# Kernel tuning notes

Measured on AMD Instinct MI355X. Metric: run time of the kernel, lower is better.

Reference implementation:

```python
import jax, jax.numpy as jnp
import numpy as np

N, E, F, H, D, C = 50000, 800000, 128, 8, 16, 40


def setup_inputs() -> dict:
    key = jax.random.key(0)
    ks = jax.random.split(key, 12)
    s_in = 1.0 / np.sqrt(F)
    s_h = 1.0 / np.sqrt(H * D)
    return {
        "x": jax.random.normal(ks[0], (N, F), jnp.float32),
        "edge_index": jax.random.randint(ks[1], (2, E), 0, N, jnp.int64),
        "W1": jax.random.normal(ks[2], (F, H * D), jnp.float32) * s_in,
        "a_src1": jax.random.normal(ks[3], (H, D), jnp.float32) * s_h,
        "a_dst1": jax.random.normal(ks[4], (H, D), jnp.float32) * s_h,
        "b1": jnp.zeros((H * D,), jnp.float32),
        "W2": jax.random.normal(ks[5], (H * D, H * D), jnp.float32) * s_h,
        "a_src2": jax.random.normal(ks[6], (H, D), jnp.float32) * s_h,
        "a_dst2": jax.random.normal(ks[7], (H, D), jnp.float32) * s_h,
        "b2": jnp.zeros((H * D,), jnp.float32),
        "Wc": jax.random.normal(ks[8], (H * D, C), jnp.float32) * s_h,
        "bc": jnp.zeros((C,), jnp.float32),
    }


def _gat_layer(x, src, dst, W, a_src, a_dst, b):
    # x: [N, F_in]; src/dst: [E'] (self-loops already appended)
    n = x.shape[0]
    h, d = a_src.shape
    hx = (x @ W).reshape(n, h, d)                      # [N, H, D]
    al_src = jnp.einsum("nhd,hd->nh", hx, a_src)       # [N, H]
    al_dst = jnp.einsum("nhd,hd->nh", hx, a_dst)       # [N, H]
    e = jax.nn.leaky_relu(al_src[src] + al_dst[dst], 0.2)  # [E', H]
    # segment softmax over incoming edges of each destination node
    m = jax.ops.segment_max(e, dst, num_segments=n)    # [N, H]
    e = jnp.exp(e - m[dst])
    z = jax.ops.segment_sum(e, dst, num_segments=n)    # [N, H]
    alpha = e / z[dst]                                 # [E', H]
    out = jax.ops.segment_sum(alpha[:, :, None] * hx[src], dst, num_segments=n)
    return out.reshape(n, h * d) + b


def reference(x, edge_index, W1, a_src1, a_dst1, b1, W2, a_src2, a_dst2, b2, Wc, bc):
    n = x.shape[0]
    loops = jnp.arange(n, dtype=edge_index.dtype)
    src = jnp.concatenate([edge_index[0], loops])  # PyG GATConv adds self-loops
    dst = jnp.concatenate([edge_index[1], loops])
    h = _gat_layer(x, src, dst, W1, a_src1, a_dst1, b1)
    h = jax.nn.elu(h)  # ELU between layers (i < K-1); dropout=None -> no-op
    h = _gat_layer(h, src, dst, W2, a_src2, a_dst2, b2)
    return h @ Wc + bc  # [N, C] logits
```

## Files before the change

kernel.cpp:

```cpp
#include <hip/hip_runtime.h>
#include <hip/hip_bf16.h>


#define FDIM 128
#define HEADS 8

typedef short bf16x8 __attribute__((ext_vector_type(8)));
typedef float f32x4 __attribute__((ext_vector_type(4)));

__device__ __forceinline__ float leaky02(float x) {
    return fmaxf(x, 0.2f * x);
}

__device__ __forceinline__ unsigned pack2bf(float x, float y) {
    unsigned a = __float_as_uint(x), b = __float_as_uint(y);
    a += 0x7fffu + ((a >> 16) & 1u);
    b += 0x7fffu + ((b >> 16) & 1u);
    return (a >> 16) | (b & 0xffff0000u);
}

__device__ __forceinline__ void split2(float x, unsigned short& hi, unsigned short& lo) {
    unsigned bits = __float_as_uint(x);
    unsigned h = bits + 0x7fffu + ((bits >> 16) & 1u);
    hi = (unsigned short)(h >> 16);
    float hf = __uint_as_float(h & 0xffff0000u);
    float r = x - hf;
    unsigned rb = __float_as_uint(r);
    unsigned l2 = rb + 0x7fffu + ((rb >> 16) & 1u);
    lo = (unsigned short)(l2 >> 16);
}


__global__ __launch_bounds__(256) void prep_kernel(const int* __restrict__ ei,
                                                   int* __restrict__ deg,
                                                   int* __restrict__ rank,
                                                   int E,
                                                   const float* __restrict__ x,
                                                   unsigned short* __restrict__ x_hi,
                                                   unsigned short* __restrict__ x_lo,
                                                   int nel,
                                                   const float* __restrict__ W1,
                                                   const float* __restrict__ W2,
                                                   unsigned short* __restrict__ w1_hi,
                                                   unsigned short* __restrict__ w1_lo,
                                                   unsigned short* __restrict__ w2_hi,
                                                   unsigned short* __restrict__ w2_lo,
                                                   int histB, int xB) {
    int b = blockIdx.x, t = threadIdx.x;
    if (b < histB) {
        int e = b * 256 + t;
        if (e < E) rank[e] = atomicAdd(&deg[ei[E + e]], 1);
        return;
    }
    b -= histB;
    if (b < xB) {
        int i0 = (b * 256 + t) * 8;
        if (i0 < nel) {
            float4 v0 = *(const float4*)&x[i0];
            float4 v1 = *(const float4*)&x[i0 + 4];
            float vv[8] = {v0.x, v0.y, v0.z, v0.w, v1.x, v1.y, v1.z, v1.w};
            unsigned short h[8], l[8];
#pragma unroll
            for (int j = 0; j < 8; ++j) split2(vv[j], h[j], l[j]);
            uint4 hh, ll;
            hh.x = h[0] | ((unsigned)h[1] << 16);
            hh.y = h[2] | ((unsigned)h[3] << 16);
            hh.z = h[4] | ((unsigned)h[5] << 16);
            hh.w = h[6] | ((unsigned)h[7] << 16);
            ll.x = l[0] | ((unsigned)l[1] << 16);
            ll.y = l[2] | ((unsigned)l[3] << 16);
            ll.z = l[4] | ((unsigned)l[5] << 16);
            ll.w = l[6] | ((unsigned)l[7] << 16);
            *(uint4*)&x_hi[i0] = hh;
            *(uint4*)&x_lo[i0] = ll;
        }
        return;
    }
    b -= xB;
    const float* W = (b < 16) ? W1 : W2;
    unsigned short* whi = (b < 16) ? w1_hi : w2_hi;
    unsigned short* wlo = (b < 16) ? w1_lo : w2_lo;
    int idx = (b & 15) * 256 + t;
    int k = idx >> 5;
    int c0 = (idx & 31) * 4;
#pragma unroll
    for (int i = 0; i < 4; ++i) {
        int c = c0 + i;
        float v = W[k * FDIM + c];
        unsigned short h, l;
        split2(v, h, l);
        int dest = ((k >> 5) * 8 + (c >> 4)) * 512 +
                   ((c & 15) + (((k >> 3) & 3) << 4)) * 8 + (k & 7);
        whi[dest] = h;
        wlo[dest] = l;
    }
}


__global__ __launch_bounds__(256) void scan_partial(const int* __restrict__ deg,
                                                    int* __restrict__ partials,
                                                    int n) {
    __shared__ int red[256];
    int t = threadIdx.x;
    int base = blockIdx.x * 1024 + t * 4;
    int s = 0;
#pragma unroll
    for (int j = 0; j < 4; ++j) {
        int i = base + j;
        if (i < n) s += deg[i];
    }
    red[t] = s;
    __syncthreads();
    for (int off = 128; off > 0; off >>= 1) {
        if (t < off) red[t] += red[t + off];
        __syncthreads();
    }
    if (t == 0) partials[blockIdx.x] = red[0];
}

__global__ __launch_bounds__(64) void scan_offsets(int* __restrict__ partials,
                                                   int* __restrict__ row_start,
                                                   int nb, int n) {
    int lane = threadIdx.x;
    int carry = 0;
    for (int base = 0; base < nb; base += 64) {
        int idx = base + lane;
        int v = (idx < nb) ? partials[idx] : 0;
        int incl = v;
#pragma unroll
        for (int off = 1; off < 64; off <<= 1) {
            int t = __shfl_up(incl, off);
            if (lane >= off) incl += t;
        }
        if (idx < nb) partials[idx] = carry + incl - v;
        carry += __shfl(incl, 63);
    }
    if (lane == 0) row_start[n] = carry;
}

__global__ __launch_bounds__(256) void scan_final(const int* __restrict__ deg,
                                                  const int* __restrict__ partials,
                                                  int* __restrict__ row_start,
                                                  int n) {
    __shared__ int sbuf[256];
    int t = threadIdx.x;
    int base = blockIdx.x * 1024 + t * 4;
    int v[4];
#pragma unroll
    for (int j = 0; j < 4; ++j) v[j] = (base + j < n) ? deg[base + j] : 0;
    int tsum = v[0] + v[1] + v[2] + v[3];
    sbuf[t] = tsum;
    __syncthreads();
    for (int off = 1; off < 256; off <<= 1) {
        int tmp = (t >= off) ? sbuf[t - off] : 0;
        __syncthreads();
        sbuf[t] += tmp;
        __syncthreads();
    }
    int toff = partials[blockIdx.x] + sbuf[t] - tsum;
    int run = 0;
#pragma unroll
    for (int j = 0; j < 4; ++j) {
        int i = base + j;
        if (i < n) row_start[i] = toff + run;
        run += v[j];
    }
}


template <bool SCATTER>
__global__ __launch_bounds__(256, 4) void gemm_mfma(const unsigned short* __restrict__ a_hi,
                                                    const unsigned short* __restrict__ a_lo,
                                                    const unsigned short* __restrict__ w_hi,
                                                    const unsigned short* __restrict__ w_lo,
                                                    const float* __restrict__ asrc,
                                                    const float* __restrict__ adst,
                                                    float* __restrict__ als,
                                                    float* __restrict__ ald,
                                                    unsigned* __restrict__ hxb,
                                                    int n,
                                                    const int* __restrict__ ei,
                                                    const int* __restrict__ rank,
                                                    const int* __restrict__ row_start,
                                                    int* __restrict__ csr_src,
                                                    int E, int ng, int grid) {
    int tid = threadIdx.x;
    int gb;
    if (SCATTER) {
        int bid = blockIdx.x;
        int t0 = (int)((long long)bid * ng / grid);
        int t1 = (int)((long long)(bid + 1) * ng / grid);
        if (t1 == t0) {
            int sb = bid - t0;
#pragma unroll
            for (int j = 0; j < 4; ++j) {
                int e = sb * 1024 + j * 256 + tid;
                if (e < E) {
                    int s = ei[e];
                    int d = ei[E + e];
                    csr_src[row_start[d] + rank[e]] = s;
                }
            }
            return;
        }
        gb = t0;
    } else {
        gb = blockIdx.x;
    }

    int lane = tid & 63;
    int wave = tid >> 6;
    int l15 = lane & 15;
    int lg = lane >> 4;
    int row0 = gb * 32;

    f32x4 acc[2][2];
#pragma unroll
    for (int fr = 0; fr < 2; ++fr)
#pragma unroll
        for (int fc = 0; fc < 2; ++fc)
#pragma unroll
            for (int r = 0; r < 4; ++r) acc[fr][fc][r] = 0.f;

#pragma unroll
    for (int kc = 0; kc < 4; ++kc) {
        bf16x8 Ah[2], Al[2], Bh[2], Bl[2];
#pragma unroll
        for (int fr = 0; fr < 2; ++fr) {
            int r = row0 + fr * 16 + l15;
            if (r > n - 1) r = n - 1;
            size_t off = (size_t)r * FDIM + kc * 32 + lg * 8;
            Ah[fr] = *(const bf16x8*)(a_hi + off);
            Al[fr] = *(const bf16x8*)(a_lo + off);
        }
#pragma unroll
        for (int fc = 0; fc < 2; ++fc) {
            int FC = wave * 2 + fc;
            size_t off = (size_t)(kc * 8 + FC) * 512 + lane * 8;
            Bh[fc] = *(const bf16x8*)(w_hi + off);
            Bl[fc] = *(const bf16x8*)(w_lo + off);
        }
#pragma unroll
        for (int fr = 0; fr < 2; ++fr)
#pragma unroll
            for (int fc = 0; fc < 2; ++fc) {
                acc[fr][fc] = __builtin_amdgcn_mfma_f32_16x16x32_bf16(
                    Al[fr], Bh[fc], acc[fr][fc], 0, 0, 0);
                acc[fr][fc] = __builtin_amdgcn_mfma_f32_16x16x32_bf16(
                    Ah[fr], Bl[fc], acc[fr][fc], 0, 0, 0);
                acc[fr][fc] = __builtin_amdgcn_mfma_f32_16x16x32_bf16(
                    Ah[fr], Bh[fc], acc[fr][fc], 0, 0, 0);
            }
    }

#pragma unroll
    for (int fr = 0; fr < 2; ++fr)
#pragma unroll
        for (int fc = 0; fc < 2; ++fc) {
            int CB = wave * 32 + fc * 16;
            int col = CB + l15;
            float as_ = asrc[col];
            float ad_ = adst[col];
#pragma unroll
            for (int reg = 0; reg < 4; ++reg) {
                int row = row0 + fr * 16 + lg * 4 + reg;
                float v = acc[fr][fc][reg];
                float vn = __shfl_xor(v, 1);
                if ((lane & 1) == 0 && row < n)
                    hxb[(size_t)row * 64 + (col >> 1)] = pack2bf(v, vn);
                float ps = v * as_;
                float pd = v * ad_;
                ps += __shfl_xor(ps, 1);
                pd += __shfl_xor(pd, 1);
                ps += __shfl_xor(ps, 2);
                pd += __shfl_xor(pd, 2);
                ps += __shfl_xor(ps, 4);
                pd += __shfl_xor(pd, 4);
                ps += __shfl_xor(ps, 8);
                pd += __shfl_xor(pd, 8);
                if (l15 == 0 && row < n) {
                    als[row * HEADS + (CB >> 4)] = ps;
                    ald[row * HEADS + (CB >> 4)] = pd;
                }
            }
        }
}


__global__ __launch_bounds__(256, 8) void gemm_cls(const unsigned* __restrict__ h_hi,
                                                   const unsigned* __restrict__ h_lo,
                                                   const float* __restrict__ W,
                                                   const float* __restrict__ bias,
                                                   float* __restrict__ out,
                                                   int n) {
    __shared__ float xs[32][136];
    __shared__ float ws[32][48];
    int tid = threadIdx.x;
    int row0 = blockIdx.x * 128;
    int lane = tid & 63;
    int wave = tid >> 6;
    int lane2 = lane * 2;
    int wc = wave * 10;

    float acc[2][10];
#pragma unroll
    for (int i = 0; i < 2; ++i)
#pragma unroll
        for (int j = 0; j < 10; ++j) acc[i][j] = 0.f;

    for (int kc = 0; kc < 128; kc += 32) {
        if (kc) __syncthreads();
#pragma unroll
        for (int it = 0; it < 4; ++it) {
            int idx = it * 256 + tid;
            int r = idx >> 3, kg = (idx & 7) * 4;
            float4 v = make_float4(0.f, 0.f, 0.f, 0.f);
            if (row0 + r < n) {
                uint2 hh = *(const uint2*)&h_hi[(size_t)(row0 + r) * 64 + (kc + kg) / 2];
                uint2 ll = *(const uint2*)&h_lo[(size_t)(row0 + r) * 64 + (kc + kg) / 2];
                v.x = __uint_as_float(hh.x << 16) + __uint_as_float(ll.x << 16);
                v.y = __uint_as_float(hh.x & 0xffff0000u) + __uint_as_float(ll.x & 0xffff0000u);
                v.z = __uint_as_float(hh.y << 16) + __uint_as_float(ll.y << 16);
                v.w = __uint_as_float(hh.y & 0xffff0000u) + __uint_as_float(ll.y & 0xffff0000u);
            }
            int col = r ^ kg;
            xs[kg + 0][col] = v.x;
            xs[kg + 1][col] = v.y;
            xs[kg + 2][col] = v.z;
            xs[kg + 3][col] = v.w;
        }
#pragma unroll
        for (int it = 0; it < 6; ++it) {
            int idx = it * 256 + tid;
            int kk = idx / 48, c = idx - kk * 48;
            ws[kk][c] = (c < 40) ? W[(size_t)(kc + kk) * 40 + c] : 0.f;
        }
        __syncthreads();
#pragma unroll
        for (int k = 0; k < 32; ++k) {
            int s = ((k >> 2) & 7) << 2;
            float2 av2 = *(const float2*)&xs[k][lane2 ^ s];
            float av[2] = {av2.x, av2.y};
#pragma unroll
            for (int j = 0; j < 10; ++j) {
                float w = ws[k][wc + j];
                acc[0][j] += av[0] * w;
                acc[1][j] += av[1] * w;
            }
        }
    }

#pragma unroll
    for (int i = 0; i < 2; ++i) {
        int row = row0 + lane2 + i;
        if (row < n) {
#pragma unroll
            for (int j = 0; j < 10; ++j)
                out[(size_t)row * 40 + wc + j] = acc[i][j] + bias[wc + j];
        }
    }
}


template <bool DOELU>
__global__ __launch_bounds__(256) void gat_aggregate(const unsigned* __restrict__ hxb,
                                                     const float* __restrict__ als,
                                                     const float* __restrict__ ald,
                                                     const int* __restrict__ row_start,
                                                     const int* __restrict__ csr_src,
                                                     const float* __restrict__ bias,
                                                     unsigned* __restrict__ h_hi,
                                                     unsigned* __restrict__ h_lo,
                                                     int n) {
    int wid = threadIdx.x >> 6;
    int lane = threadIdx.x & 63;
    int node = blockIdx.x * 4 + wid;
    if (node >= n) return;

    int rs = row_start[node];
    int deg = row_start[node + 1] - rs;

    int h = lane & 7;
    int hc = lane >> 3;
    float ald_h = ald[node * HEADS + h];

    float acc0 = 0.f, acc1 = 0.f, z = 0.f;
    int total = deg + 1;
    int i0 = 0;
    for (; i0 + 8 <= total; i0 += 8) {
        int ii = i0 + (lane >> 3);
        int srcv = (ii < deg) ? csr_src[rs + ii] : node;
        float w = __expf(leaky02(als[srcv * HEADS + h] + ald_h));
#pragma unroll
        for (int e = 0; e < 8; ++e) {
            int s    = __shfl(srcv, e * 8);
            float we = __shfl(w, e * 8 + hc);
            unsigned v = hxb[(size_t)s * 64 + lane];
            z += we;
            acc0 += we * __uint_as_float(v << 16);
            acc1 += we * __uint_as_float(v & 0xffff0000u);
        }
    }
    {
        int ii = i0 + (lane >> 3);
        int srcv = (ii < deg) ? csr_src[rs + ii] : node;
        float w = (ii < total) ? __expf(leaky02(als[srcv * HEADS + h] + ald_h)) : 0.f;
        int rem = total - i0;
        for (int e = 0; e < rem; ++e) {
            int s    = __shfl(srcv, e * 8);
            float we = __shfl(w, e * 8 + hc);
            unsigned v = hxb[(size_t)s * 64 + lane];
            z += we;
            acc0 += we * __uint_as_float(v << 16);
            acc1 += we * __uint_as_float(v & 0xffff0000u);
        }
    }

    float2 bv = *(const float2*)&bias[2 * lane];
    float o0 = acc0 / z + bv.x;
    float o1 = acc1 / z + bv.y;
    if (DOELU) {
        o0 = o0 > 0.f ? o0 : (__expf(o0) - 1.f);
        o1 = o1 > 0.f ? o1 : (__expf(o1) - 1.f);
    }
    unsigned short h0, l0, h1, l1;
    split2(o0, h0, l0);
    split2(o1, h1, l1);
    h_hi[(size_t)node * 64 + lane] = (unsigned)h0 | ((unsigned)h1 << 16);
    h_lo[(size_t)node * 64 + lane] = (unsigned)l0 | ((unsigned)l1 << 16);
}


extern "C" void kernel_launch(void* const* d_in, const int* in_sizes, int n_in,
                              void* d_out, int out_size, void* d_ws, size_t ws_size,
                              hipStream_t stream) {
    const float* x      = (const float*)d_in[0];
    const int*   ei     = (const int*)d_in[1];
    const float* W1     = (const float*)d_in[2];
    const float* a_src1 = (const float*)d_in[3];
    const float* a_dst1 = (const float*)d_in[4];
    const float* b1     = (const float*)d_in[5];
    const float* W2     = (const float*)d_in[6];
    const float* a_src2 = (const float*)d_in[7];
    const float* a_dst2 = (const float*)d_in[8];
    const float* b2     = (const float*)d_in[9];
    const float* Wc     = (const float*)d_in[10];
    const float* bc     = (const float*)d_in[11];
    float* out = (float*)d_out;

    const int N = in_sizes[0] / FDIM;
    const int E = in_sizes[1] / 2;
    const int NB = (N + 1023) / 1024;
    const int nel = N * FDIM;

    unsigned* hxb = (unsigned*)d_ws;
    unsigned* xh_u = hxb + (size_t)N * 64;
    unsigned* xl_u = xh_u + (size_t)N * 64;
    float* als  = (float*)(xl_u + (size_t)N * 64);
    float* ald  = als + (size_t)N * HEADS;
    unsigned short* w1_hi = (unsigned short*)(ald + (size_t)N * HEADS);
    unsigned short* w1_lo = w1_hi + 16384;
    unsigned short* w2_hi = w1_lo + 16384;
    unsigned short* w2_lo = w2_hi + 16384;
    int* deg       = (int*)(w2_lo + 16384);
    int* row_start = deg + N;
    int* partials  = row_start + ((N + 8) & ~3);
    int* rank      = partials + ((NB + 4) & ~3);
    int* csr_src   = rank + E;

    unsigned short* x_hi = (unsigned short*)xh_u;
    unsigned short* x_lo = (unsigned short*)xl_u;

    hipMemsetAsync(deg, 0, (size_t)N * sizeof(int), stream);
    const int histB = (E + 255) / 256;
    const int xB = (nel + 2047) / 2048;
    prep_kernel<<<histB + xB + 32, 256, 0, stream>>>(
        ei, deg, rank, E, x, x_hi, x_lo, nel,
        W1, W2, w1_hi, w1_lo, w2_hi, w2_lo, histB, xB);
    scan_partial<<<NB, 256, 0, stream>>>(deg, partials, N);
    scan_offsets<<<1, 64, 0, stream>>>(partials, row_start, NB, N);
    scan_final<<<NB, 256, 0, stream>>>(deg, partials, row_start, N);

    const int ng = (N + 31) / 32;
    const int ns = (E + 1023) / 1024;
    const int grid1 = ng + ns;
    const int agg_grid = (N + 3) / 4;
    const int cls_grid = (N + 127) / 128;

    gemm_mfma<true><<<grid1, 256, 0, stream>>>(x_hi, x_lo, w1_hi, w1_lo,
                                               a_src1, a_dst1, als, ald, hxb, N,
                                               ei, rank, row_start, csr_src,
                                               E, ng, grid1);
    gat_aggregate<true><<<agg_grid, 256, 0, stream>>>(hxb, als, ald, row_start,
                                                      csr_src, b1, xh_u, xl_u, N);
    gemm_mfma<false><<<ng, 256, 0, stream>>>(x_hi, x_lo, w2_hi, w2_lo,
                                             a_src2, a_dst2, als, ald, hxb, N,
                                             nullptr, nullptr, nullptr, nullptr,
                                             0, ng, ng);
    gat_aggregate<false><<<agg_grid, 256, 0, stream>>>(hxb, als, ald, row_start,
                                                       csr_src, b2, xh_u, xl_u, N);
    gemm_cls<<<cls_grid, 256, 0, stream>>>(xh_u, xl_u, Wc, bc, out, N);
}
```

Measured before the change: 235.7 us.

## Split each node's edge aggregation across two waves and drop final lo-part output

The aggregation kernel now assigns two waves per destination node, each processing half of the incoming edges, and combines the partial sums and normalizer through shared memory before writing. This targets latency-bound per-node gathers by doubling parallelism per node. The second layer now writes only a single bf16 result instead of a hi/lo split pair, and the classifier GEMM reads only the hi part. That cuts memory traffic but lowers the precision of the classifier input. The extra block-wide barrier and shared-memory reduction add some overhead.

```diff
diff --git a/kernel.cpp b/kernel.cpp
--- a/kernel.cpp
+++ b/kernel.cpp
@@ -288,7 +288,6 @@
 
 
 __global__ __launch_bounds__(256, 8) void gemm_cls(const unsigned* __restrict__ h_hi,
-                                                   const unsigned* __restrict__ h_lo,
                                                    const float* __restrict__ W,
                                                    const float* __restrict__ bias,
                                                    float* __restrict__ out,
@@ -317,11 +316,10 @@
             float4 v = make_float4(0.f, 0.f, 0.f, 0.f);
             if (row0 + r < n) {
                 uint2 hh = *(const uint2*)&h_hi[(size_t)(row0 + r) * 64 + (kc + kg) / 2];
-                uint2 ll = *(const uint2*)&h_lo[(size_t)(row0 + r) * 64 + (kc + kg) / 2];
-                v.x = __uint_as_float(hh.x << 16) + __uint_as_float(ll.x << 16);
-                v.y = __uint_as_float(hh.x & 0xffff0000u) + __uint_as_float(ll.x & 0xffff0000u);
-                v.z = __uint_as_float(hh.y << 16) + __uint_as_float(ll.y << 16);
-                v.w = __uint_as_float(hh.y & 0xffff0000u) + __uint_as_float(ll.y & 0xffff0000u);
+                v.x = __uint_as_float(hh.x << 16);
+                v.y = __uint_as_float(hh.x & 0xffff0000u);
+                v.z = __uint_as_float(hh.y << 16);
+                v.w = __uint_as_float(hh.y & 0xffff0000u);
             }
             int col = r ^ kg;
             xs[kg + 0][col] = v.x;
@@ -362,7 +360,7 @@
 }
 
 
-template <bool DOELU>
+template <bool DOELU, bool WRITELO>
 __global__ __launch_bounds__(256) void gat_aggregate(const unsigned* __restrict__ hxb,
                                                      const float* __restrict__ als,
                                                      const float* __restrict__ ald,
@@ -372,22 +370,31 @@
                                                      unsigned* __restrict__ h_hi,
                                                      unsigned* __restrict__ h_lo,
                                                      int n) {
-    int wid = threadIdx.x >> 6;
-    int lane = threadIdx.x & 63;
-    int node = blockIdx.x * 4 + wid;
-    if (node >= n) return;
-
-    int rs = row_start[node];
-    int deg = row_start[node + 1] - rs;
+    __shared__ float part[256 * 3];
+    int tid = threadIdx.x;
+    int wave = tid >> 6;
+    int lane = tid & 63;
+    int node = blockIdx.x * 2 + (wave >> 1);
+    int half = wave & 1;
+    bool valid = node < n;
+
+    int rs = 0, deg = 0;
+    if (valid) {
+        rs = row_start[node];
+        deg = row_start[node + 1] - rs;
+    }
+    int total = deg + 1;
+    int mid = (total + 1) >> 1;
+    int start = valid ? (half ? mid : 0) : 0;
+    int end   = valid ? (half ? total : mid) : 0;
 
     int h = lane & 7;
     int hc = lane >> 3;
-    float ald_h = ald[node * HEADS + h];
+    float ald_h = valid ? ald[node * HEADS + h] : 0.f;
 
     float acc0 = 0.f, acc1 = 0.f, z = 0.f;
-    int total = deg + 1;
-    int i0 = 0;
-    for (; i0 + 8 <= total; i0 += 8) {
+    int i0 = start;
+    for (; i0 + 8 <= end; i0 += 8) {
         int ii = i0 + (lane >> 3);
         int srcv = (ii < deg) ? csr_src[rs + ii] : node;
         float w = __expf(leaky02(als[srcv * HEADS + h] + ald_h));
@@ -401,11 +408,12 @@
             acc1 += we * __uint_as_float(v & 0xffff0000u);
         }
     }
-    {
+    if (i0 < end) {
         int ii = i0 + (lane >> 3);
-        int srcv = (ii < deg) ? csr_src[rs + ii] : node;
-        float w = (ii < total) ? __expf(leaky02(als[srcv * HEADS + h] + ald_h)) : 0.f;
-        int rem = total - i0;
+        int srcv = node;
+        if (ii < deg) srcv = csr_src[rs + ii];
+        float w = (ii < end && valid) ? __expf(leaky02(als[srcv * HEADS + h] + ald_h)) : 0.f;
+        int rem = end - i0;
         for (int e = 0; e < rem; ++e) {
             int s    = __shfl(srcv, e * 8);
             float we = __shfl(w, e * 8 + hc);
@@ -416,18 +424,33 @@
         }
     }
 
-    float2 bv = *(const float2*)&bias[2 * lane];
-    float o0 = acc0 / z + bv.x;
-    float o1 = acc1 / z + bv.y;
-    if (DOELU) {
-        o0 = o0 > 0.f ? o0 : (__expf(o0) - 1.f);
-        o1 = o1 > 0.f ? o1 : (__expf(o1) - 1.f);
-    }
-    unsigned short h0, l0, h1, l1;
-    split2(o0, h0, l0);
-    split2(o1, h1, l1);
-    h_hi[(size_t)node * 64 + lane] = (unsigned)h0 | ((unsigned)h1 << 16);
-    h_lo[(size_t)node * 64 + lane] = (unsigned)l0 | ((unsigned)l1 << 16);
+    float* mine = part + tid * 3;
+    mine[0] = acc0;
+    mine[1] = acc1;
+    mine[2] = z;
+    __syncthreads();
+    if (half == 0 && valid) {
+        const float* other = part + ((wave ^ 1) * 64 + lane) * 3;
+        acc0 += other[0];
+        acc1 += other[1];
+        z    += other[2];
+        float2 bv = *(const float2*)&bias[2 * lane];
+        float o0 = acc0 / z + bv.x;
+        float o1 = acc1 / z + bv.y;
+        if (DOELU) {
+            o0 = o0 > 0.f ? o0 : (__expf(o0) - 1.f);
+            o1 = o1 > 0.f ? o1 : (__expf(o1) - 1.f);
+        }
+        if (WRITELO) {
+            unsigned short h0, l0, h1, l1;
+            split2(o0, h0, l0);
+            split2(o1, h1, l1);
+            h_hi[(size_t)node * 64 + lane] = (unsigned)h0 | ((unsigned)h1 << 16);
+            h_lo[(size_t)node * 64 + lane] = (unsigned)l0 | ((unsigned)l1 << 16);
+        } else {
+            h_hi[(size_t)node * 64 + lane] = pack2bf(o0, o1);
+        }
+    }
 }
 
 
@@ -484,20 +507,20 @@
     const int ng = (N + 31) / 32;
     const int ns = (E + 1023) / 1024;
     const int grid1 = ng + ns;
-    const int agg_grid = (N + 3) / 4;
+    const int agg_grid = (N + 1) / 2;
     const int cls_grid = (N + 127) / 128;
 
     gemm_mfma<true><<<grid1, 256, 0, stream>>>(x_hi, x_lo, w1_hi, w1_lo,
                                                a_src1, a_dst1, als, ald, hxb, N,
                                                ei, rank, row_start, csr_src,
                                                E, ng, grid1);
-    gat_aggregate<true><<<agg_grid, 256, 0, stream>>>(hxb, als, ald, row_start,
-                                                      csr_src, b1, xh_u, xl_u, N);
+    gat_aggregate<true, true><<<agg_grid, 256, 0, stream>>>(
+        hxb, als, ald, row_start, csr_src, b1, xh_u, xl_u, N);
     gemm_mfma<false><<<ng, 256, 0, stream>>>(x_hi, x_lo, w2_hi, w2_lo,
                                              a_src2, a_dst2, als, ald, hxb, N,
                                              nullptr, nullptr, nullptr, nullptr,
                                              0, ng, ng);
-    gat_aggregate<false><<<agg_grid, 256, 0, stream>>>(hxb, als, ald, row_start,
-                                                       csr_src, b2, xh_u, xl_u, N);
-    gemm_cls<<<cls_grid, 256, 0, stream>>>(xh_u, xl_u, Wc, bc, out, N);
-}
+    gat_aggregate<false, false><<<agg_grid, 256, 0, stream>>>(
+        hxb, als, ald, row_start, csr_src, b2, xh_u, xl_u, N);
+    gemm_cls<<<cls_grid, 256, 0, stream>>>(xh_u, Wc, bc, out, N);
+}
```

After: 255.9 us. 8.6% more time.

## Store aggregation features in fp16 and drop lo-part write for final layer

Applied to the files above, without the earlier changes.

Switches the gathered per-node feature buffer from bf16 to fp16 for better precision, and makes the second aggregation write a single fp16 buffer instead of a hi/lo bf16 pair, so the classifier reads half the bytes. The softmax denominator is now summed once per edge group with a few shuffles instead of inside the inner loop. It also marks the CSR scatter stores as nontemporal. fp16 has less range than bf16, which risks overflow on large activations.

```diff
diff --git a/kernel.cpp b/kernel.cpp
--- a/kernel.cpp
+++ b/kernel.cpp
@@ -1,5 +1,6 @@
 #include <hip/hip_runtime.h>
 #include <hip/hip_bf16.h>
+#include <hip/hip_fp16.h>
 
 
 #define FDIM 128
@@ -12,11 +13,9 @@
     return fmaxf(x, 0.2f * x);
 }
 
-__device__ __forceinline__ unsigned pack2bf(float x, float y) {
-    unsigned a = __float_as_uint(x), b = __float_as_uint(y);
-    a += 0x7fffu + ((a >> 16) & 1u);
-    b += 0x7fffu + ((b >> 16) & 1u);
-    return (a >> 16) | (b & 0xffff0000u);
+__device__ __forceinline__ unsigned pack2h(float x, float y) {
+    __half2 h2 = __floats2half2_rn(x, y);
+    return *(unsigned*)&h2;
 }
 
 __device__ __forceinline__ void split2(float x, unsigned short& hi, unsigned short& lo) {
@@ -177,7 +176,7 @@
                                                     const float* __restrict__ adst,
                                                     float* __restrict__ als,
                                                     float* __restrict__ ald,
-                                                    unsigned* __restrict__ hxb,
+                                                    unsigned* __restrict__ hxf,
                                                     int n,
                                                     const int* __restrict__ ei,
                                                     const int* __restrict__ rank,
@@ -198,7 +197,7 @@
                 if (e < E) {
                     int s = ei[e];
                     int d = ei[E + e];
-                    csr_src[row_start[d] + rank[e]] = s;
+                    __builtin_nontemporal_store(s, &csr_src[row_start[d] + rank[e]]);
                 }
             }
             return;
@@ -267,7 +266,7 @@
                 float v = acc[fr][fc][reg];
                 float vn = __shfl_xor(v, 1);
                 if ((lane & 1) == 0 && row < n)
-                    hxb[(size_t)row * 64 + (col >> 1)] = pack2bf(v, vn);
+                    hxf[(size_t)row * 64 + (col >> 1)] = pack2h(v, vn);
                 float ps = v * as_;
                 float pd = v * ad_;
                 ps += __shfl_xor(ps, 1);
@@ -287,8 +286,7 @@
 }
 
 
-__global__ __launch_bounds__(256, 8) void gemm_cls(const unsigned* __restrict__ h_hi,
-                                                   const unsigned* __restrict__ h_lo,
+__global__ __launch_bounds__(256, 8) void gemm_cls(const unsigned* __restrict__ h_f16,
                                                    const float* __restrict__ W,
                                                    const float* __restrict__ bias,
                                                    float* __restrict__ out,
@@ -316,12 +314,10 @@
             int r = idx >> 3, kg = (idx & 7) * 4;
             float4 v = make_float4(0.f, 0.f, 0.f, 0.f);
             if (row0 + r < n) {
-                uint2 hh = *(const uint2*)&h_hi[(size_t)(row0 + r) * 64 + (kc + kg) / 2];
-                uint2 ll = *(const uint2*)&h_lo[(size_t)(row0 + r) * 64 + (kc + kg) / 2];
-                v.x = __uint_as_float(hh.x << 16) + __uint_as_float(ll.x << 16);
-                v.y = __uint_as_float(hh.x & 0xffff0000u) + __uint_as_float(ll.x & 0xffff0000u);
-                v.z = __uint_as_float(hh.y << 16) + __uint_as_float(ll.y << 16);
-                v.w = __uint_as_float(hh.y & 0xffff0000u) + __uint_as_float(ll.y & 0xffff0000u);
+                uint2 hh = *(const uint2*)&h_f16[(size_t)(row0 + r) * 64 + (kc + kg) / 2];
+                float2 a = __half22float2(*(__half2*)&hh.x);
+                float2 b = __half22float2(*(__half2*)&hh.y);
+                v.x = a.x; v.y = a.y; v.z = b.x; v.w = b.y;
             }
             int col = r ^ kg;
             xs[kg + 0][col] = v.x;
@@ -362,8 +358,8 @@
 }
 
 
-template <bool DOELU>
-__global__ __launch_bounds__(256) void gat_aggregate(const unsigned* __restrict__ hxb,
+template <bool DOELU, bool WRITELO>
+__global__ __launch_bounds__(256) void gat_aggregate(const unsigned* __restrict__ hxf,
                                                      const float* __restrict__ als,
                                                      const float* __restrict__ ald,
                                                      const int* __restrict__ row_start,
@@ -384,37 +380,44 @@
     int hc = lane >> 3;
     float ald_h = ald[node * HEADS + h];
 
-    float acc0 = 0.f, acc1 = 0.f, z = 0.f;
+    float acc0 = 0.f, acc1 = 0.f, zown = 0.f;
     int total = deg + 1;
     int i0 = 0;
     for (; i0 + 8 <= total; i0 += 8) {
         int ii = i0 + (lane >> 3);
         int srcv = (ii < deg) ? csr_src[rs + ii] : node;
         float w = __expf(leaky02(als[srcv * HEADS + h] + ald_h));
+        zown += w;
 #pragma unroll
         for (int e = 0; e < 8; ++e) {
             int s    = __shfl(srcv, e * 8);
             float we = __shfl(w, e * 8 + hc);
-            unsigned v = hxb[(size_t)s * 64 + lane];
-            z += we;
-            acc0 += we * __uint_as_float(v << 16);
-            acc1 += we * __uint_as_float(v & 0xffff0000u);
+            unsigned v = hxf[(size_t)s * 64 + lane];
+            float2 f = __half22float2(*(__half2*)&v);
+            acc0 += we * f.x;
+            acc1 += we * f.y;
         }
     }
     {
         int ii = i0 + (lane >> 3);
         int srcv = (ii < deg) ? csr_src[rs + ii] : node;
         float w = (ii < total) ? __expf(leaky02(als[srcv * HEADS + h] + ald_h)) : 0.f;
+        zown += w;
         int rem = total - i0;
         for (int e = 0; e < rem; ++e) {
             int s    = __shfl(srcv, e * 8);
             float we = __shfl(w, e * 8 + hc);
-            unsigned v = hxb[(size_t)s * 64 + lane];
-            z += we;
-            acc0 += we * __uint_as_float(v << 16);
-            acc1 += we * __uint_as_float(v & 0xffff0000u);
-        }
-    }
+            unsigned v = hxf[(size_t)s * 64 + lane];
+            float2 f = __half22float2(*(__half2*)&v);
+            acc0 += we * f.x;
+            acc1 += we * f.y;
+        }
+    }
+
+    zown += __shfl_xor(zown, 8);
+    zown += __shfl_xor(zown, 16);
+    zown += __shfl_xor(zown, 32);
+    float z = __shfl(zown, hc);
 
     float2 bv = *(const float2*)&bias[2 * lane];
     float o0 = acc0 / z + bv.x;
@@ -423,11 +426,15 @@
         o0 = o0 > 0.f ? o0 : (__expf(o0) - 1.f);
         o1 = o1 > 0.f ? o1 : (__expf(o1) - 1.f);
     }
-    unsigned short h0, l0, h1, l1;
-    split2(o0, h0, l0);
-    split2(o1, h1, l1);
-    h_hi[(size_t)node * 64 + lane] = (unsigned)h0 | ((unsigned)h1 << 16);
-    h_lo[(size_t)node * 64 + lane] = (unsigned)l0 | ((unsigned)l1 << 16);
+    if (WRITELO) {
+        unsigned short hh0, ll0, hh1, ll1;
+        split2(o0, hh0, ll0);
+        split2(o1, hh1, ll1);
+        h_hi[(size_t)node * 64 + lane] = (unsigned)hh0 | ((unsigned)hh1 << 16);
+        h_lo[(size_t)node * 64 + lane] = (unsigned)ll0 | ((unsigned)ll1 << 16);
+    } else {
+        h_hi[(size_t)node * 64 + lane] = pack2h(o0, o1);
+    }
 }
 
 
@@ -453,8 +460,8 @@
     const int NB = (N + 1023) / 1024;
     const int nel = N * FDIM;
 
-    unsigned* hxb = (unsigned*)d_ws;
-    unsigned* xh_u = hxb + (size_t)N * 64;
+    unsigned* hxf = (unsigned*)d_ws;
+    unsigned* xh_u = hxf + (size_t)N * 64;
     unsigned* xl_u = xh_u + (size_t)N * 64;
     float* als  = (float*)(xl_u + (size_t)N * 64);
     float* ald  = als + (size_t)N * HEADS;
@@ -488,16 +495,16 @@
     const int cls_grid = (N + 127) / 128;
 
     gemm_mfma<true><<<grid1, 256, 0, stream>>>(x_hi, x_lo, w1_hi, w1_lo,
-                                               a_src1, a_dst1, als, ald, hxb, N,
+                                               a_src1, a_dst1, als, ald, hxf, N,
                                                ei, rank, row_start, csr_src,
                                                E, ng, grid1);
-    gat_aggregate<true><<<agg_grid, 256, 0, stream>>>(hxb, als, ald, row_start,
-                                                      csr_src, b1, xh_u, xl_u, N);
+    gat_aggregate<true, true><<<agg_grid, 256, 0, stream>>>(
+        hxf, als, ald, row_start, csr_src, b1, xh_u, xl_u, N);
     gemm_mfma<false><<<ng, 256, 0, stream>>>(x_hi, x_lo, w2_hi, w2_lo,
-                                             a_src2, a_dst2, als, ald, hxb, N,
+                                             a_src2, a_dst2, als, ald, hxf, N,
                                              nullptr, nullptr, nullptr, nullptr,
                                              0, ng, ng);
-    gat_aggregate<false><<<agg_grid, 256, 0, stream>>>(hxb, als, ald, row_start,
-                                                       csr_src, b2, xh_u, xl_u, N);
-    gemm_cls<<<cls_grid, 256, 0, stream>>>(xh_u, xl_u, Wc, bc, out, N);
-}
+    gat_aggregate<false, false><<<agg_grid, 256, 0, stream>>>(
+        hxf, als, ald, row_start, csr_src, b2, xh_u, xl_u, N);
+    gemm_cls<<<cls_grid, 256, 0, stream>>>(xh_u, Wc, bc, out, N);
+}
```

After: 233.8 us. No clear change (-0.8%).
